# Kernel optimization log

Measured on AMD Instinct MI355X. Metric: run time of the kernel, lower is better.

Reference implementation:

```python
import jax, jax.numpy as jnp
import numpy as np

RCUT = 6.0      # cutoff radius
AXIS = 16       # axis_neuron
NORM = 64.0     # normalizer = avg_neighbors + 1 (precomputed stat)
EPS = 1e-15
NTYPES = 2


def _embed(h, W0, b0, W1, b1, W2, b2):
    # tiny per-type-pair embedding MLP: scalar sr -> C channels
    h = jnp.tanh(h @ W0 + b0)
    h = jnp.tanh(h @ W1 + b1)
    return jnp.tanh(h @ W2 + b2)


def _forward(coord_3N, box_33, srmean, srstd, xrsrstd, Gbias, Ebias,
             emb_W0, emb_b0, emb_W1, emb_b1, emb_W2, emb_b2,
             fit_W0, fit_b0, fit_W1, fit_b1, fit_W2, fit_b2, n1):
    N = coord_3N.shape[1]
    L = jnp.diagonal(box_33)  # orthorhombic box lengths (3,)
    # relative coords with minimum-image convention: x[d,i,j] = c[d,j] - c[d,i]
    x_3NM = coord_3N[:, None, :] - coord_3N[:, :, None]
    x_3NM = x_3NM - L[:, None, None] * jnp.round(x_3NM / L[:, None, None])
    eye = jnp.eye(N, dtype=bool)
    r_NM = jnp.sqrt(jnp.where(eye, 1.0, (x_3NM ** 2).sum(0)))  # diag masked for safe grad
    # smooth switching / r  (DeepPot-SE style sr)
    u = r_NM / RCUT
    sw = jnp.where((r_NM < RCUT) & (~eye), ((-6.0 * u + 15.0) * u - 10.0) * u ** 3 + 1.0, 0.0)
    sr_NM = sw / r_NM
    rsr_NM = sr_NM / r_NM
    idx = (0, n1, N)  # contiguous type boundaries (atoms sorted by type)
    rows_sr, rows_rsr, rows_emb = [], [], []
    for i in range(NTYPES):
        sr_i = sr_NM[idx[i]:idx[i + 1]]
        rows_sr.append(sr_i / srstd[i])
        rows_rsr.append(rsr_NM[idx[i]:idx[i + 1]] / xrsrstd[i])
        srn_i = (sr_i - srmean[i]) / srstd[i]
        blocks = []
        for j in range(NTYPES):
            p = NTYPES * i + j  # type-pair index
            blocks.append(_embed(srn_i[:, idx[j]:idx[j + 1], None],
                                 emb_W0[p], emb_b0[p], emb_W1[p], emb_b1[p], emb_W2[p], emb_b2[p]))
        rows_emb.append(jnp.concatenate(blocks, axis=1))
    srbias_NM = jnp.concatenate(rows_sr, axis=0)
    R_3NM = (jnp.concatenate(rows_rsr, axis=0)[None] + EPS) * x_3NM  # e3norm = 1
    embed_NMC = jnp.concatenate(rows_emb, axis=0)
    # weighted reductions over neighbor axis M (einsum avoids the 3*N*M*C temp)
    Ginv_NC = jnp.einsum('nm,nmc->nc', srbias_NM, embed_NMC) / NORM
    Geqv_3NC = jnp.einsum('dnm,nmc->dnc', R_3NM, embed_NMC) / NORM
    G_4NC = jnp.concatenate([(Ginv_NC + Gbias)[None], Geqv_3NC], axis=0)
    # equivariant outer-product descriptor: Feat[n,a,c] = sum_k G[k,n,c]*G[k,n,a]
    Feat_NX = jnp.einsum('knc,kna->nac', G_4NC, G_4NC[:, :, :AXIS]).reshape(N, -1)
    energy = jnp.zeros((), dtype=Feat_NX.dtype)
    for i in range(NTYPES):
        h = Feat_NX[idx[i]:idx[i + 1]]
        h = jnp.tanh(h @ fit_W0[i] + fit_b0[i])
        h = jnp.tanh(h @ fit_W1[i] + fit_b1[i])
        h = h @ fit_W2[i] + fit_b2[i]
        energy = energy + (h + Ebias[i]).sum()
    return energy


def setup_inputs() -> dict:
    key = jax.random.key(0)
    ks = jax.random.split(key, 20)
    N, N1, BOXL = 1024, 512, 20.0
    W = (16, 32, 64)
    X, F = AXIS * W[-1], 128

    def wt(k, shape, fan_in):
        return jax.random.normal(k, shape, jnp.float32) / np.float32(np.sqrt(fan_in))

    return {
        'coord_3N': jax.random.uniform(ks[0], (3, N), jnp.float32) * BOXL,
        'box_33': BOXL * jnp.eye(3, dtype=jnp.float32),
        'srmean': 0.1 * jax.random.uniform(ks[1], (NTYPES,), jnp.float32),
        'srstd': 0.5 + jax.random.uniform(ks[2], (NTYPES,), jnp.float32),
        'xrsrstd': 0.5 + jax.random.uniform(ks[3], (NTYPES,), jnp.float32),
        'Gbias': 0.1 * jax.random.normal(ks[4], (W[2],), jnp.float32),
        'Ebias': jax.random.normal(ks[5], (NTYPES,), jnp.float32),
        'emb_W0': wt(ks[6], (4, 1, W[0]), 1),
        'emb_b0': 0.1 * jax.random.normal(ks[7], (4, W[0]), jnp.float32),
        'emb_W1': wt(ks[8], (4, W[0], W[1]), W[0]),
        'emb_b1': 0.1 * jax.random.normal(ks[9], (4, W[1]), jnp.float32),
        'emb_W2': wt(ks[10], (4, W[1], W[2]), W[1]),
        'emb_b2': 0.1 * jax.random.normal(ks[11], (4, W[2]), jnp.float32),
        'fit_W0': wt(ks[12], (NTYPES, X, F), X),
        'fit_b0': 0.1 * jax.random.normal(ks[13], (NTYPES, F), jnp.float32),
        'fit_W1': wt(ks[14], (NTYPES, F, F), F),
        'fit_b1': 0.1 * jax.random.normal(ks[15], (NTYPES, F), jnp.float32),
        'fit_W2': wt(ks[16], (NTYPES, F, 1), F),
        'fit_b2': 0.1 * jax.random.normal(ks[17], (NTYPES, 1), jnp.float32),
        'n1': N1,
    }


def reference(coord_3N, box_33, srmean, srstd, xrsrstd, Gbias, Ebias,
              emb_W0, emb_b0, emb_W1, emb_b1, emb_W2, emb_b2,
              fit_W0, fit_b0, fit_W1, fit_b1, fit_W2, fit_b2, n1):
    return _forward(coord_3N, box_33, srmean, srstd, xrsrstd, Gbias, Ebias,
                    emb_W0, emb_b0, emb_W1, emb_b1, emb_W2, emb_b2,
                    fit_W0, fit_b0, fit_W1, fit_b1, fit_W2, fit_b2, n1)
```

## Files before the change

kernel.cpp:

```cpp
#include <hip/hip_runtime.h>

#define RCUT 6.0f

typedef _Float16 h2v __attribute__((ext_vector_type(2)));
typedef _Float16 h8  __attribute__((ext_vector_type(8)));
typedef float    f4  __attribute__((ext_vector_type(4)));

__device__ __forceinline__ float fast_tanh(float x) {
    float e = __expf(2.0f * x);
    return 1.0f - 2.0f * __builtin_amdgcn_rcpf(e + 1.0f);
}

__device__ __forceinline__ h2v pkh(float a, float b) {
#if __has_builtin(__builtin_amdgcn_cvt_pkrtz)
    union { __fp16 __attribute__((ext_vector_type(2))) r; h2v h; } u;
    u.r = __builtin_amdgcn_cvt_pkrtz(a, b);
    return u.h;
#else
    h2v r; r.x = (_Float16)a; r.y = (_Float16)b; return r;
#endif
}

__global__ __launch_bounds__(256, 2) void k_embed(
    const float* __restrict__ coord, const float* __restrict__ box,
    const float* __restrict__ srmean, const float* __restrict__ srstd,
    const float* __restrict__ xrsrstd, const float* __restrict__ Gbias,
    const float* __restrict__ eW0, const float* __restrict__ eb0,
    const float* __restrict__ eW1, const float* __restrict__ eb1,
    const float* __restrict__ eW2, const float* __restrict__ eb2,
    const int* __restrict__ n1p,
    const float* __restrict__ fW0, const float* __restrict__ fW1,
    h2v* __restrict__ feat, _Float16* __restrict__ W0ht,
    _Float16* __restrict__ W1ht, unsigned int* __restrict__ counter, int N)
{
    const int nb  = blockIdx.x;
    const int tid = threadIdx.x;
    const int NB  = N >> 1;

    __shared__ float s_w0[2][16], s_b0[2][16];
    __shared__ __align__(16) _Float16 s_srn[1024];
    __shared__ __align__(16) _Float16 s_cf[4][1024];
    __shared__ __align__(16) _Float16 s_h1[128][32];
    __shared__ __align__(16) _Float16 s_ef[4][4][64][8];
    __shared__ unsigned short s_nbr[1024];
    __shared__ float s_g4[2][256];
    __shared__ __align__(16) _Float16 w1t[2][32][24];
    __shared__ __align__(16) _Float16 w2t[2][64][40];
    __shared__ int s_wA[4], s_wB[4];

    if (nb >= NB) {
        const int b = nb - NB;
        if (b == 0 && tid == 0) *counter = 0u;
        float (*s_t)[33] = reinterpret_cast<float(*)[33]>(&s_ef[0][0][0][0]);
        if (b < 256) {
            int type = b >> 7, tb = b & 127;
            int ki = tb >> 2, ci = tb & 3;
            const float* src = fW0 + (size_t)type * 131072;
            int c = tid & 31, r0 = (tid >> 5) * 4;
            #pragma unroll
            for (int q = 0; q < 4; q++)
                s_t[r0 + q][c] = src[(size_t)(ki * 32 + r0 + q) * 128 + ci * 32 + c];
            __syncthreads();
            _Float16* dst = W0ht + (size_t)type * 131072;
            int kk = tid & 31, c0 = (tid >> 5) * 4;
            #pragma unroll
            for (int q = 0; q < 4; q++)
                dst[(size_t)(ci * 32 + c0 + q) * 1024 + ki * 32 + kk] = (_Float16)s_t[kk][c0 + q];
        } else {
            int b2v = b - 256, type = b2v >> 4, tb = b2v & 15;
            int ki = tb >> 2, ci = tb & 3;
            const float* src = fW1 + (size_t)type * 16384;
            int c = tid & 31, r0 = (tid >> 5) * 4;
            #pragma unroll
            for (int q = 0; q < 4; q++)
                s_t[r0 + q][c] = src[(size_t)(ki * 32 + r0 + q) * 128 + ci * 32 + c];
            __syncthreads();
            _Float16* dst = W1ht + (size_t)type * 16384;
            int kk = tid & 31, c0 = (tid >> 5) * 4;
            #pragma unroll
            for (int q = 0; q < 4; q++)
                dst[(size_t)(ci * 32 + c0 + q) * 128 + ki * 32 + kk] = (_Float16)s_t[kk][c0 + q];
        }
        return;
    }

    const int nA = 2 * nb, nBt = 2 * nb + 1;
    const int n1 = *n1p;
    const int ti = (nA >= n1) ? 1 : 0;
    const int wid = tid >> 6, lane = tid & 63;
    const int l15 = lane & 15, lk = lane >> 4;

    for (int t = tid; t < 32; t += 256) { int j = t >> 4, f = t & 15;
        s_w0[j][f] = eW0[(2 * ti + j) * 16 + f];
        s_b0[j][f] = eb0[(2 * ti + j) * 16 + f]; }
    for (int idx = tid; idx < 1024; idx += 256) {
        int j = idx >> 9, r = idx & 511, f = r >> 5, g = r & 31;
        w1t[j][g][f] = (_Float16)eW1[(2 * ti + j) * 512 + f * 32 + g];
    }
    for (int idx = tid; idx < 4096; idx += 256) {
        int j = idx >> 11, r = idx & 2047, g = r >> 6, c = r & 63;
        w2t[j][c][g] = (_Float16)eW2[(2 * ti + j) * 2048 + g * 64 + c];
    }
    float b1r[2][2], b2r[2][4];
    #pragma unroll
    for (int j = 0; j < 2; j++) {
        #pragma unroll
        for (int q = 0; q < 2; q++) b1r[j][q] = eb1[(2 * ti + j) * 32 + 16 * q + l15];
        #pragma unroll
        for (int q = 0; q < 4; q++) b2r[j][q] = eb2[(2 * ti + j) * 64 + 16 * q + l15];
    }

    const float Lx = box[0], Ly = box[4], Lz = box[8];
    const float iLx = 1.0f / Lx, iLy = 1.0f / Ly, iLz = 1.0f / Lz;
    const float xA = coord[nA], yA = coord[N + nA], zA = coord[2 * N + nA];
    const float xB = coord[nBt], yB = coord[N + nBt], zB = coord[2 * N + nBt];
    const float srm  = srmean[ti];
    const float isrs = 1.0f / srstd[ti];
    const float ixrs = 1.0f / xrsrstd[ti];

    unsigned long long balA[4], balB[4];
    {
        int wA = 0, wB = 0;
        const int mystart = wid * 256;
        #pragma unroll
        for (int r = 0; r < 4; r++) {
            int m = mystart + r * 64 + lane;
            float x = coord[m], y = coord[N + m], z = coord[2 * N + m];
            float ax = x - xA; ax -= Lx * rintf(ax * iLx);
            float ay = y - yA; ay -= Ly * rintf(ay * iLy);
            float az = z - zA; az -= Lz * rintf(az * iLz);
            float ra = ax * ax + ay * ay + az * az;
            float bx = x - xB; bx -= Lx * rintf(bx * iLx);
            float by = y - yB; by -= Ly * rintf(by * iLy);
            float bz = z - zB; bz -= Lz * rintf(bz * iLz);
            float rb = bx * bx + by * by + bz * bz;
            bool pA = (ra < RCUT * RCUT) && (m != nA);
            bool pB = (rb < RCUT * RCUT) && (m != nBt);
            balA[r] = __ballot(pA);
            balB[r] = __ballot(pB);
            wA += (int)__popcll(balA[r]);
            wB += (int)__popcll(balB[r]);
        }
        if (lane == 0) { s_wA[wid] = wA; s_wB[wid] = wB; }
    }
    __syncthreads();
    int cntA = s_wA[0] + s_wA[1] + s_wA[2] + s_wA[3];
    int cntB = s_wB[0] + s_wB[1] + s_wB[2] + s_wB[3];
    int cnt  = cntA + cntB;
    if (cnt > 1024) cnt = 1024;
    if (cntA > 1024) cntA = 1024;
    {
        int baseA = 0, baseB = cntA;
        for (int w = 0; w < wid; w++) { baseA += s_wA[w]; baseB += s_wB[w]; }
        const unsigned long long lt = (1ull << lane) - 1ull;
        const int mystart = wid * 256;
        #pragma unroll
        for (int r = 0; r < 4; r++) {
            int m = mystart + r * 64 + lane;
            float x = coord[m], y = coord[N + m], z = coord[2 * N + m];
            #pragma unroll
            for (int cc = 0; cc < 2; cc++) {
                unsigned long long bal = cc ? balB[r] : balA[r];
                int base = cc ? baseB : baseA;
                if ((bal >> lane) & 1ull) {
                    int pos = base + (int)__popcll(bal & lt);
                    if (pos < 1024) {
                        float dx = x - (cc ? xB : xA); dx -= Lx * rintf(dx * iLx);
                        float dy = y - (cc ? yB : yA); dy -= Ly * rintf(dy * iLy);
                        float dz = z - (cc ? zB : zA); dz -= Lz * rintf(dz * iLz);
                        float r2 = dx * dx + dy * dy + dz * dz;
                        float rr = sqrtf(r2);
                        float rinv = __builtin_amdgcn_rcpf(rr);
                        float u  = rr * (1.0f / RCUT);
                        float u3 = u * u * u;
                        float sw_ = ((-6.0f * u + 15.0f) * u - 10.0f) * u3 + 1.0f;
                        float sr  = sw_ * rinv;
                        float crs = sr * rinv * ixrs + 1e-15f;
                        s_srn[pos]   = (_Float16)((sr - srm) * isrs);
                        s_cf[0][pos] = (_Float16)(sr * isrs);
                        s_cf[1][pos] = (_Float16)(crs * dx);
                        s_cf[2][pos] = (_Float16)(crs * dy);
                        s_cf[3][pos] = (_Float16)(crs * dz);
                        s_nbr[pos]   = (unsigned short)m;
                    }
                }
                if (cc) baseB += (int)__popcll(bal);
                else    baseA += (int)__popcll(bal);
            }
        }
    }
    __syncthreads();
    const int ntiles = (cnt + 127) >> 7;
    for (int i = cnt + tid; i < ntiles * 128; i += 256) {
        s_srn[i] = (_Float16)0.0f; s_nbr[i] = 0;
        s_cf[0][i] = (_Float16)0.0f; s_cf[1][i] = (_Float16)0.0f;
        s_cf[2][i] = (_Float16)0.0f; s_cf[3][i] = (_Float16)0.0f;
    }
    __syncthreads();

    f4 gacc = {0.0f, 0.0f, 0.0f, 0.0f};
    const f4 zf4 = {0.0f, 0.0f, 0.0f, 0.0f};

    for (int t = 0; t < ntiles; t++) {
        const int t128 = t << 7;
        __syncthreads();

        #pragma unroll
        for (int mt2 = 0; mt2 < 2; mt2++) {
            const int mt = 2 * wid + mt2;
            const int row = 16 * mt + l15;
            const int rp = t128 + row;
            float srn = (float)s_srn[rp];
            int jr = (s_nbr[rp] >= n1) ? 1 : 0;
            h8 a = {};
            if (lk < 2) {
                const float* wp = &s_w0[jr][8 * lk];
                const float* bp = &s_b0[jr][8 * lk];
                #pragma unroll
                for (int q = 0; q < 8; q++)
                    a[q] = (_Float16)fast_tanh(fmaf(srn, wp[q], bp[q]));
            }
            #pragma unroll
            for (int nt1 = 0; nt1 < 2; nt1++) {
                const int c = 16 * nt1 + l15;
                h8 b0f = {}, b1f = {};
                if (lk < 2) {
                    b0f = *(const h8*)&w1t[0][c][8 * lk];
                    b1f = *(const h8*)&w1t[1][c][8 * lk];
                }
                f4 d0 = __builtin_amdgcn_mfma_f32_16x16x32_f16(a, b0f, zf4, 0, 0, 0);
                f4 d1 = __builtin_amdgcn_mfma_f32_16x16x32_f16(a, b1f, zf4, 0, 0, 0);
                #pragma unroll
                for (int r = 0; r < 4; r++) {
                    int gp = 16 * mt + 4 * lk + r;
                    bool is0 = (s_nbr[t128 + gp] < n1);
                    float hv = fast_tanh((is0 ? d0[r] : d1[r]) + (is0 ? b1r[0][nt1] : b1r[1][nt1]));
                    int e = 16 * nt1 + l15;
                    s_h1[gp][(((e >> 3) ^ ((gp >> 1) & 3)) << 3) + (e & 7)] = (_Float16)hv;
                }
            }
        }
        asm volatile("" ::: "memory");
        #pragma unroll
        for (int mt2 = 0; mt2 < 2; mt2++) {
            const int mt = 2 * wid + mt2;
            const int row = 16 * mt + l15;
            h8 a2 = *(const h8*)&s_h1[row][((lk ^ ((row >> 1) & 3)) << 3)];
            #pragma unroll
            for (int nt = 0; nt < 4; nt++) {
                const int c = 16 * nt + l15;
                h8 w20 = *(const h8*)&w2t[0][c][8 * lk];
                h8 w21 = *(const h8*)&w2t[1][c][8 * lk];
                f4 e0 = __builtin_amdgcn_mfma_f32_16x16x32_f16(a2, w20, zf4, 0, 0, 0);
                f4 e1 = __builtin_amdgcn_mfma_f32_16x16x32_f16(a2, w21, zf4, 0, 0, 0);
                #pragma unroll
                for (int r = 0; r < 4; r++) {
                    int gp = 16 * mt + 4 * lk + r;
                    bool is0 = (s_nbr[t128 + gp] < n1);
                    float ev = fast_tanh((is0 ? e0[r] : e1[r]) + (is0 ? b2r[0][nt] : b2r[1][nt]));
                    s_ef[nt][gp >> 5][l15 + 16 * ((gp & 31) >> 3)][gp & 7] = (_Float16)ev;
                }
            }
        }
        __syncthreads();

        #pragma unroll
        for (int ks = 0; ks < 4; ks++) {
            const int s = t128 + 32 * ks;
            h8 ac = {};
            if (l15 < 8) {
                const bool rowA = l15 < 4;
                const int  cr   = rowA ? l15 : (l15 - 4);
                const bool allA = (s + 31) < cntA;
                const bool allB = s >= cntA;
                if ((allA && rowA) || (allB && !rowA)) {
                    ac = *(const h8*)&s_cf[cr][s + 8 * lk];
                } else if (!allA && !allB) {
                    #pragma unroll
                    for (int r = 0; r < 8; r++) {
                        int p = s + 8 * lk + r;
                        bool isA = p < cntA;
                        if (isA == rowA) ac[r] = s_cf[cr][p];
                    }
                }
            }
            h8 eb = *(const h8*)&s_ef[wid][ks][lane][0];
            gacc = __builtin_amdgcn_mfma_f32_16x16x32_f16(ac, eb, gacc, 0, 0, 0);
        }
    }

    if (lk < 2) {
        float* sg = &s_g4[lk][0];
        #pragma unroll
        for (int r = 0; r < 4; r++) {
            float gv = gacc[r] * (1.0f / 64.0f);
            if (r == 0) gv += Gbias[16 * wid + l15];
            sg[r * 64 + 16 * wid + l15] = gv;
        }
    }
    __syncthreads();
    #pragma unroll
    for (int at = 0; at < 2; at++) {
        const float* sg = &s_g4[at][0];
        h2v* outp = feat + (size_t)(2 * nb + at) * 512;
        #pragma unroll
        for (int q = 0; q < 2; q++) {
            int o2 = tid + 256 * q;
            int a = o2 >> 5, c = (2 * o2) & 63;
            float ga0 = sg[a],       ga1 = sg[64 + a];
            float ga2 = sg[128 + a], ga3 = sg[192 + a];
            float s0 = ga0 * sg[c];
            s0 = fmaf(ga1, sg[64 + c],  s0);
            s0 = fmaf(ga2, sg[128 + c], s0);
            s0 = fmaf(ga3, sg[192 + c], s0);
            float s1 = ga0 * sg[c + 1];
            s1 = fmaf(ga1, sg[64 + c + 1],  s1);
            s1 = fmaf(ga2, sg[128 + c + 1], s1);
            s1 = fmaf(ga3, sg[192 + c + 1], s1);
            outp[o2] = pkh(s0, s1);
        }
    }
}

__global__ __launch_bounds__(512) void k_fit(
    const _Float16* __restrict__ featf, const _Float16* __restrict__ W0ht,
    const _Float16* __restrict__ W1ht,
    const float* __restrict__ b0, const float* __restrict__ b1,
    const float* __restrict__ W2, const float* __restrict__ b2,
    const float* __restrict__ Ebias, const int* __restrict__ n1p,
    unsigned int* __restrict__ counter, float* __restrict__ slots,
    float* __restrict__ out)
{
    __shared__ float s_red[4][2][16][64];
    __shared__ __align__(16) _Float16 s_hd[16][128];
    __shared__ float s_sum[16][32];

    const int tid = threadIdx.x;
    const int lane = tid & 63, w = tid >> 6;
    const int kq = w >> 1, ch = w & 1;
    const int l15 = lane & 15, lk = lane >> 4;
    const int n0 = blockIdx.x * 16;
    const int ia = (n0 >= *n1p) ? 1 : 0;
    const f4 zf4 = {0.0f, 0.0f, 0.0f, 0.0f};

    const _Float16* Ap = featf + (size_t)(n0 + l15) * 1024 + kq * 256;
    const _Float16* B0 = W0ht + (size_t)ia * 131072 + kq * 256;
    f4 acc[4] = {zf4, zf4, zf4, zf4};
    #pragma unroll
    for (int ks = 0; ks < 8; ks++) {
        h8 a = *(const h8*)(Ap + ks * 32 + 8 * lk);
        #pragma unroll
        for (int nt = 0; nt < 4; nt++) {
            const int c = ch * 64 + nt * 16 + l15;
            h8 b = *(const h8*)(B0 + (size_t)c * 1024 + ks * 32 + 8 * lk);
            acc[nt] = __builtin_amdgcn_mfma_f32_16x16x32_f16(a, b, acc[nt], 0, 0, 0);
        }
    }
    #pragma unroll
    for (int nt = 0; nt < 4; nt++)
        #pragma unroll
        for (int r = 0; r < 4; r++)
            s_red[kq][ch][4 * lk + r][nt * 16 + l15] = acc[nt][r];
    __syncthreads();

    {
        const int row = tid >> 5, c0 = (tid & 31) * 4;
        const int chh = c0 >> 6, cl = c0 & 63;
        f4 v = *(const f4*)&s_red[0][chh][row][cl];
        v += *(const f4*)&s_red[1][chh][row][cl];
        v += *(const f4*)&s_red[2][chh][row][cl];
        v += *(const f4*)&s_red[3][chh][row][cl];
        #pragma unroll
        for (int q = 0; q < 4; q++) {
            int c = c0 + q;
            float h = fast_tanh(v[q] + b0[ia * 128 + c]);
            s_hd[row][(((c >> 3) ^ row) << 3) + (c & 7)] = (_Float16)h;
        }
    }
    __syncthreads();

    f4 acc1[4] = {zf4, zf4, zf4, zf4};
    {
        h8 a = *(const h8*)&s_hd[l15][(((4 * kq + lk) ^ l15) & 15) << 3];
        const _Float16* B1 = W1ht + (size_t)ia * 16384 + kq * 32;
        #pragma unroll
        for (int nt = 0; nt < 4; nt++) {
            const int c = ch * 64 + nt * 16 + l15;
            h8 b = *(const h8*)(B1 + (size_t)c * 128 + 8 * lk);
            acc1[nt] = __builtin_amdgcn_mfma_f32_16x16x32_f16(a, b, zf4, 0, 0, 0);
        }
    }
    #pragma unroll
    for (int nt = 0; nt < 4; nt++)
        #pragma unroll
        for (int r = 0; r < 4; r++)
            s_red[kq][ch][4 * lk + r][nt * 16 + l15] = acc1[nt][r];
    __syncthreads();

    {
        const int row = tid >> 5, c0 = (tid & 31) * 4;
        const int chh = c0 >> 6, cl = c0 & 63;
        f4 v = *(const f4*)&s_red[0][chh][row][cl];
        v += *(const f4*)&s_red[1][chh][row][cl];
        v += *(const f4*)&s_red[2][chh][row][cl];
        v += *(const f4*)&s_red[3][chh][row][cl];
        float pv = 0.0f;
        #pragma unroll
        for (int q = 0; q < 4; q++) {
            int c = c0 + q;
            pv += fast_tanh(v[q] + b1[ia * 128 + c]) * W2[ia * 128 + c];
        }
        s_sum[row][tid & 31] = pv;
    }
    __syncthreads();
    if (w == 0) {
        const int row = lane >> 2, g = lane & 3;
        float s = 0.0f;
        #pragma unroll
        for (int i = 0; i < 8; i++) s += s_sum[row][8 * g + i];
        s += __shfl_xor(s, 1);  s += __shfl_xor(s, 2);
        s += __shfl_xor(s, 4);  s += __shfl_xor(s, 8);
        s += __shfl_xor(s, 16); s += __shfl_xor(s, 32);
        if (lane == 0) {
            float e = s + 16.0f * (b2[ia] + Ebias[ia]);
            slots[blockIdx.x] = e;
            __threadfence();
            unsigned int old = atomicAdd(counter, 1u);
            if (old == 63u) {
                __threadfence();
                float tot = 0.0f;
                for (int i = 0; i < 64; i++)
                    tot += __hip_atomic_load(&slots[i], __ATOMIC_RELAXED, __HIP_MEMORY_SCOPE_AGENT);
                out[0] = tot;
            }
        }
    }
}

extern "C" void kernel_launch(void* const* d_in, const int* in_sizes, int n_in,
                              void* d_out, int out_size, void* d_ws, size_t ws_size,
                              hipStream_t stream) {
    const float* coord   = (const float*)d_in[0];
    const float* box     = (const float*)d_in[1];
    const float* srmean  = (const float*)d_in[2];
    const float* srstd   = (const float*)d_in[3];
    const float* xrsrstd = (const float*)d_in[4];
    const float* Gbias   = (const float*)d_in[5];
    const float* Ebias   = (const float*)d_in[6];
    const float* eW0     = (const float*)d_in[7];
    const float* eb0     = (const float*)d_in[8];
    const float* eW1     = (const float*)d_in[9];
    const float* eb1     = (const float*)d_in[10];
    const float* eW2     = (const float*)d_in[11];
    const float* eb2     = (const float*)d_in[12];
    const float* fW0     = (const float*)d_in[13];
    const float* fb0     = (const float*)d_in[14];
    const float* fW1     = (const float*)d_in[15];
    const float* fb1     = (const float*)d_in[16];
    const float* fW2     = (const float*)d_in[17];
    const float* fb2     = (const float*)d_in[18];
    const int*   n1p     = (const int*)d_in[19];

    const int N = in_sizes[0] / 3;
    h2v*      featbuf = (h2v*)d_ws;
    _Float16* W0ht = (_Float16*)((char*)d_ws + (size_t)2 * 1024 * 1024);
    _Float16* W1ht = W0ht + 2 * 131072;
    char* tail = (char*)d_ws + (size_t)(2 * 1024 + 512 + 64) * 1024;
    unsigned int* counter = (unsigned int*)tail;
    float*        slots   = (float*)(tail + 64);

    k_embed<<<N / 2 + 288, 256, 0, stream>>>(coord, box, srmean, srstd, xrsrstd,
                                             Gbias, eW0, eb0, eW1, eb1, eW2, eb2,
                                             n1p, fW0, fW1, featbuf, W0ht, W1ht,
                                             counter, N);
    k_fit<<<N / 16, 512, 0, stream>>>((const _Float16*)featbuf, W0ht, W1ht,
                                      fb0, fb1, fW2, fb2, Ebias, n1p,
                                      counter, slots, (float*)d_out);
}
```

Before: 39.37 us.

## Process one atom per block and accumulate G in registers instead of MFMA

```diff
diff --git a/kernel.cpp b/kernel.cpp
--- a/kernel.cpp
+++ b/kernel.cpp
@@ -21,7 +21,7 @@
 #endif
 }
 
-__global__ __launch_bounds__(256, 2) void k_embed(
+__global__ __launch_bounds__(256, 4) void k_embed(
     const float* __restrict__ coord, const float* __restrict__ box,
     const float* __restrict__ srmean, const float* __restrict__ srstd,
     const float* __restrict__ xrsrstd, const float* __restrict__ Gbias,
@@ -33,25 +33,23 @@
     h2v* __restrict__ feat, _Float16* __restrict__ W0ht,
     _Float16* __restrict__ W1ht, unsigned int* __restrict__ counter, int N)
 {
-    const int nb  = blockIdx.x;
     const int tid = threadIdx.x;
-    const int NB  = N >> 1;
 
     __shared__ float s_w0[2][16], s_b0[2][16];
-    __shared__ __align__(16) _Float16 s_srn[1024];
-    __shared__ __align__(16) _Float16 s_cf[4][1024];
+    __shared__ __align__(16) _Float16 s_srn[512];
+    __shared__ __align__(16) _Float16 s_cf[4][512];
     __shared__ __align__(16) _Float16 s_h1[128][32];
-    __shared__ __align__(16) _Float16 s_ef[4][4][64][8];
-    __shared__ unsigned short s_nbr[1024];
-    __shared__ float s_g4[2][256];
+    __shared__ unsigned short s_nbr[512];
+    __shared__ float s_g[4][4][64];
+    __shared__ float s_g4[256];
     __shared__ __align__(16) _Float16 w1t[2][32][24];
     __shared__ __align__(16) _Float16 w2t[2][64][40];
-    __shared__ int s_wA[4], s_wB[4];
-
-    if (nb >= NB) {
-        const int b = nb - NB;
+    __shared__ int s_wcnt[4];
+
+    if (blockIdx.x >= (unsigned)N) {
+        const int b = blockIdx.x - N;
         if (b == 0 && tid == 0) *counter = 0u;
-        float (*s_t)[33] = reinterpret_cast<float(*)[33]>(&s_ef[0][0][0][0]);
+        float (*s_t)[33] = reinterpret_cast<float(*)[33]>(&s_h1[0][0]);
         if (b < 256) {
             int type = b >> 7, tb = b & 127;
             int ki = tb >> 2, ci = tb & 3;
@@ -84,9 +82,9 @@
         return;
     }
 
-    const int nA = 2 * nb, nBt = 2 * nb + 1;
+    const int n  = blockIdx.x;
     const int n1 = *n1p;
-    const int ti = (nA >= n1) ? 1 : 0;
+    const int ti = (n >= n1) ? 1 : 0;
     const int wid = tid >> 6, lane = tid & 63;
     const int l15 = lane & 15, lk = lane >> 4;
 
@@ -112,81 +110,62 @@
 
     const float Lx = box[0], Ly = box[4], Lz = box[8];
     const float iLx = 1.0f / Lx, iLy = 1.0f / Ly, iLz = 1.0f / Lz;
-    const float xA = coord[nA], yA = coord[N + nA], zA = coord[2 * N + nA];
-    const float xB = coord[nBt], yB = coord[N + nBt], zB = coord[2 * N + nBt];
+    const float xn = coord[n], yn = coord[N + n], zn = coord[2 * N + n];
     const float srm  = srmean[ti];
     const float isrs = 1.0f / srstd[ti];
     const float ixrs = 1.0f / xrsrstd[ti];
 
-    unsigned long long balA[4], balB[4];
-    {
-        int wA = 0, wB = 0;
+    unsigned long long bal[4];
+    {
+        int wc = 0;
         const int mystart = wid * 256;
         #pragma unroll
         for (int r = 0; r < 4; r++) {
             int m = mystart + r * 64 + lane;
-            float x = coord[m], y = coord[N + m], z = coord[2 * N + m];
-            float ax = x - xA; ax -= Lx * rintf(ax * iLx);
-            float ay = y - yA; ay -= Ly * rintf(ay * iLy);
-            float az = z - zA; az -= Lz * rintf(az * iLz);
-            float ra = ax * ax + ay * ay + az * az;
-            float bx = x - xB; bx -= Lx * rintf(bx * iLx);
-            float by = y - yB; by -= Ly * rintf(by * iLy);
-            float bz = z - zB; bz -= Lz * rintf(bz * iLz);
-            float rb = bx * bx + by * by + bz * bz;
-            bool pA = (ra < RCUT * RCUT) && (m != nA);
-            bool pB = (rb < RCUT * RCUT) && (m != nBt);
-            balA[r] = __ballot(pA);
-            balB[r] = __ballot(pB);
-            wA += (int)__popcll(balA[r]);
-            wB += (int)__popcll(balB[r]);
-        }
-        if (lane == 0) { s_wA[wid] = wA; s_wB[wid] = wB; }
-    }
-    __syncthreads();
-    int cntA = s_wA[0] + s_wA[1] + s_wA[2] + s_wA[3];
-    int cntB = s_wB[0] + s_wB[1] + s_wB[2] + s_wB[3];
-    int cnt  = cntA + cntB;
-    if (cnt > 1024) cnt = 1024;
-    if (cntA > 1024) cntA = 1024;
-    {
-        int baseA = 0, baseB = cntA;
-        for (int w = 0; w < wid; w++) { baseA += s_wA[w]; baseB += s_wB[w]; }
+            float dx = coord[m] - xn;         dx -= Lx * rintf(dx * iLx);
+            float dy = coord[N + m] - yn;     dy -= Ly * rintf(dy * iLy);
+            float dz = coord[2 * N + m] - zn; dz -= Lz * rintf(dz * iLz);
+            float r2 = dx * dx + dy * dy + dz * dz;
+            bool pred = (r2 < RCUT * RCUT) && (m != n);
+            bal[r] = __ballot(pred);
+            wc += (int)__popcll(bal[r]);
+        }
+        if (lane == 0) s_wcnt[wid] = wc;
+    }
+    __syncthreads();
+    int cnt = s_wcnt[0] + s_wcnt[1] + s_wcnt[2] + s_wcnt[3];
+    if (cnt > 512) cnt = 512;
+    {
+        int base = 0;
+        for (int w = 0; w < wid; w++) base += s_wcnt[w];
         const unsigned long long lt = (1ull << lane) - 1ull;
         const int mystart = wid * 256;
         #pragma unroll
         for (int r = 0; r < 4; r++) {
             int m = mystart + r * 64 + lane;
-            float x = coord[m], y = coord[N + m], z = coord[2 * N + m];
-            #pragma unroll
-            for (int cc = 0; cc < 2; cc++) {
-                unsigned long long bal = cc ? balB[r] : balA[r];
-                int base = cc ? baseB : baseA;
-                if ((bal >> lane) & 1ull) {
-                    int pos = base + (int)__popcll(bal & lt);
-                    if (pos < 1024) {
-                        float dx = x - (cc ? xB : xA); dx -= Lx * rintf(dx * iLx);
-                        float dy = y - (cc ? yB : yA); dy -= Ly * rintf(dy * iLy);
-                        float dz = z - (cc ? zB : zA); dz -= Lz * rintf(dz * iLz);
-                        float r2 = dx * dx + dy * dy + dz * dz;
-                        float rr = sqrtf(r2);
-                        float rinv = __builtin_amdgcn_rcpf(rr);
-                        float u  = rr * (1.0f / RCUT);
-                        float u3 = u * u * u;
-                        float sw_ = ((-6.0f * u + 15.0f) * u - 10.0f) * u3 + 1.0f;
-                        float sr  = sw_ * rinv;
-                        float crs = sr * rinv * ixrs + 1e-15f;
-                        s_srn[pos]   = (_Float16)((sr - srm) * isrs);
-                        s_cf[0][pos] = (_Float16)(sr * isrs);
-                        s_cf[1][pos] = (_Float16)(crs * dx);
-                        s_cf[2][pos] = (_Float16)(crs * dy);
-                        s_cf[3][pos] = (_Float16)(crs * dz);
-                        s_nbr[pos]   = (unsigned short)m;
-                    }
+            if ((bal[r] >> lane) & 1ull) {
+                int pos = base + (int)__popcll(bal[r] & lt);
+                if (pos < 512) {
+                    float dx = coord[m] - xn;         dx -= Lx * rintf(dx * iLx);
+                    float dy = coord[N + m] - yn;     dy -= Ly * rintf(dy * iLy);
+                    float dz = coord[2 * N + m] - zn; dz -= Lz * rintf(dz * iLz);
+                    float r2 = dx * dx + dy * dy + dz * dz;
+                    float rr = sqrtf(r2);
+                    float rinv = __builtin_amdgcn_rcpf(rr);
+                    float u  = rr * (1.0f / RCUT);
+                    float u3 = u * u * u;
+                    float sw_ = ((-6.0f * u + 15.0f) * u - 10.0f) * u3 + 1.0f;
+                    float sr  = sw_ * rinv;
+                    float crs = sr * rinv * ixrs + 1e-15f;
+                    s_srn[pos]   = (_Float16)((sr - srm) * isrs);
+                    s_cf[0][pos] = (_Float16)(sr * isrs);
+                    s_cf[1][pos] = (_Float16)(crs * dx);
+                    s_cf[2][pos] = (_Float16)(crs * dy);
+                    s_cf[3][pos] = (_Float16)(crs * dz);
+                    s_nbr[pos]   = (unsigned short)m;
                 }
-                if (cc) baseB += (int)__popcll(bal);
-                else    baseA += (int)__popcll(bal);
-            }
+            }
+            base += (int)__popcll(bal[r]);
         }
     }
     __syncthreads();
@@ -198,13 +177,11 @@
     }
     __syncthreads();
 
-    f4 gacc = {0.0f, 0.0f, 0.0f, 0.0f};
     const f4 zf4 = {0.0f, 0.0f, 0.0f, 0.0f};
+    float gk[4][4] = {};
 
     for (int t = 0; t < ntiles; t++) {
         const int t128 = t << 7;
-        __syncthreads();
-
         #pragma unroll
         for (int mt2 = 0; mt2 < 2; mt2++) {
             const int mt = 2 * wid + mt2;
@@ -220,6 +197,11 @@
                 for (int q = 0; q < 8; q++)
                     a[q] = (_Float16)fast_tanh(fmaf(srn, wp[q], bp[q]));
             }
+            int j_r[4];
+            #pragma unroll
+            for (int r = 0; r < 4; r++)
+                j_r[r] = (s_nbr[t128 + 16 * mt + 4 * lk + r] >= n1) ? 1 : 0;
+
             #pragma unroll
             for (int nt1 = 0; nt1 < 2; nt1++) {
                 const int c = 16 * nt1 + l15;
@@ -233,90 +215,74 @@
                 #pragma unroll
                 for (int r = 0; r < 4; r++) {
                     int gp = 16 * mt + 4 * lk + r;
-                    bool is0 = (s_nbr[t128 + gp] < n1);
-                    float hv = fast_tanh((is0 ? d0[r] : d1[r]) + (is0 ? b1r[0][nt1] : b1r[1][nt1]));
+                    float hv = fast_tanh((j_r[r] ? d1[r] : d0[r]) + (j_r[r] ? b1r[1][nt1] : b1r[0][nt1]));
                     int e = 16 * nt1 + l15;
                     s_h1[gp][(((e >> 3) ^ ((gp >> 1) & 3)) << 3) + (e & 7)] = (_Float16)hv;
                 }
             }
-        }
-        asm volatile("" ::: "memory");
-        #pragma unroll
-        for (int mt2 = 0; mt2 < 2; mt2++) {
-            const int mt = 2 * wid + mt2;
-            const int row = 16 * mt + l15;
+            asm volatile("" ::: "memory");
+
             h8 a2 = *(const h8*)&s_h1[row][((lk ^ ((row >> 1) & 3)) << 3)];
+            float cfv[4][4];
+            #pragma unroll
+            for (int k = 0; k < 4; k++) {
+                #pragma unroll
+                for (int r = 0; r < 4; r++)
+                    cfv[k][r] = (float)s_cf[k][t128 + 16 * mt + 4 * lk + r];
+            }
             #pragma unroll
             for (int nt = 0; nt < 4; nt++) {
-                const int c = 16 * nt + l15;
-                h8 w20 = *(const h8*)&w2t[0][c][8 * lk];
-                h8 w21 = *(const h8*)&w2t[1][c][8 * lk];
+                h8 w20 = *(const h8*)&w2t[0][16 * nt + l15][8 * lk];
+                h8 w21 = *(const h8*)&w2t[1][16 * nt + l15][8 * lk];
                 f4 e0 = __builtin_amdgcn_mfma_f32_16x16x32_f16(a2, w20, zf4, 0, 0, 0);
                 f4 e1 = __builtin_amdgcn_mfma_f32_16x16x32_f16(a2, w21, zf4, 0, 0, 0);
                 #pragma unroll
                 for (int r = 0; r < 4; r++) {
-                    int gp = 16 * mt + 4 * lk + r;
-                    bool is0 = (s_nbr[t128 + gp] < n1);
-                    float ev = fast_tanh((is0 ? e0[r] : e1[r]) + (is0 ? b2r[0][nt] : b2r[1][nt]));
-                    s_ef[nt][gp >> 5][l15 + 16 * ((gp & 31) >> 3)][gp & 7] = (_Float16)ev;
+                    float ev = fast_tanh((j_r[r] ? e1[r] : e0[r]) + (j_r[r] ? b2r[1][nt] : b2r[0][nt]));
+                    #pragma unroll
+                    for (int k = 0; k < 4; k++)
+                        gk[k][nt] = fmaf(cfv[k][r], ev, gk[k][nt]);
                 }
             }
         }
-        __syncthreads();
-
-        #pragma unroll
-        for (int ks = 0; ks < 4; ks++) {
-            const int s = t128 + 32 * ks;
-            h8 ac = {};
-            if (l15 < 8) {
-                const bool rowA = l15 < 4;
-                const int  cr   = rowA ? l15 : (l15 - 4);
-                const bool allA = (s + 31) < cntA;
-                const bool allB = s >= cntA;
-                if ((allA && rowA) || (allB && !rowA)) {
-                    ac = *(const h8*)&s_cf[cr][s + 8 * lk];
-                } else if (!allA && !allB) {
-                    #pragma unroll
-                    for (int r = 0; r < 8; r++) {
-                        int p = s + 8 * lk + r;
-                        bool isA = p < cntA;
-                        if (isA == rowA) ac[r] = s_cf[cr][p];
-                    }
-                }
-            }
-            h8 eb = *(const h8*)&s_ef[wid][ks][lane][0];
-            gacc = __builtin_amdgcn_mfma_f32_16x16x32_f16(ac, eb, gacc, 0, 0, 0);
-        }
-    }
-
-    if (lk < 2) {
-        float* sg = &s_g4[lk][0];
-        #pragma unroll
-        for (int r = 0; r < 4; r++) {
-            float gv = gacc[r] * (1.0f / 64.0f);
-            if (r == 0) gv += Gbias[16 * wid + l15];
-            sg[r * 64 + 16 * wid + l15] = gv;
-        }
-    }
-    __syncthreads();
+    }
+
     #pragma unroll
-    for (int at = 0; at < 2; at++) {
-        const float* sg = &s_g4[at][0];
-        h2v* outp = feat + (size_t)(2 * nb + at) * 512;
+    for (int k = 0; k < 4; k++) {
+        #pragma unroll
+        for (int nt = 0; nt < 4; nt++) {
+            float v = gk[k][nt];
+            v += __shfl_xor(v, 16);
+            v += __shfl_xor(v, 32);
+            if (lane < 16) s_g[wid][k][nt * 16 + lane] = v;
+        }
+    }
+    __syncthreads();
+    {
+        int k = tid >> 6, c = tid & 63;
+        float g = (s_g[0][k][c] + s_g[1][k][c]) + (s_g[2][k][c] + s_g[3][k][c]);
+        g *= (1.0f / 64.0f);
+        if (k == 0) g += Gbias[c];
+        s_g4[k * 64 + c] = g;
+    }
+    __syncthreads();
+
+    {
+        h2v* outp = feat + (size_t)n * 512;
         #pragma unroll
         for (int q = 0; q < 2; q++) {
             int o2 = tid + 256 * q;
             int a = o2 >> 5, c = (2 * o2) & 63;
-            float ga0 = sg[a],       ga1 = sg[64 + a];
-            float ga2 = sg[128 + a], ga3 = sg[192 + a];
-            float s0 = ga0 * sg[c];
-            s0 = fmaf(ga1, sg[64 + c],  s0);
-            s0 = fmaf(ga2, sg[128 + c], s0);
-            s0 = fmaf(ga3, sg[192 + c], s0);
-            float s1 = ga0 * sg[c + 1];
-            s1 = fmaf(ga1, sg[64 + c + 1],  s1);
-            s1 = fmaf(ga2, sg[128 + c + 1], s1);
-            s1 = fmaf(ga3, sg[192 + c + 1], s1);
+            float ga0 = s_g4[a],       ga1 = s_g4[64 + a];
+            float ga2 = s_g4[128 + a], ga3 = s_g4[192 + a];
+            float s0 = ga0 * s_g4[c];
+            s0 = fmaf(ga1, s_g4[64 + c],  s0);
+            s0 = fmaf(ga2, s_g4[128 + c], s0);
+            s0 = fmaf(ga3, s_g4[192 + c], s0);
+            float s1 = ga0 * s_g4[c + 1];
+            s1 = fmaf(ga1, s_g4[64 + c + 1],  s1);
+            s1 = fmaf(ga2, s_g4[128 + c + 1], s1);
+            s1 = fmaf(ga3, s_g4[192 + c + 1], s1);
             outp[o2] = pkh(s0, s1);
         }
     }
@@ -469,10 +435,10 @@
     unsigned int* counter = (unsigned int*)tail;
     float*        slots   = (float*)(tail + 64);
 
-    k_embed<<<N / 2 + 288, 256, 0, stream>>>(coord, box, srmean, srstd, xrsrstd,
-                                             Gbias, eW0, eb0, eW1, eb1, eW2, eb2,
-                                             n1p, fW0, fW1, featbuf, W0ht, W1ht,
-                                             counter, N);
+    k_embed<<<N + 288, 256, 0, stream>>>(coord, box, srmean, srstd, xrsrstd,
+                                         Gbias, eW0, eb0, eW1, eb1, eW2, eb2,
+                                         n1p, fW0, fW1, featbuf, W0ht, W1ht,
+                                         counter, N);
     k_fit<<<N / 16, 512, 0, stream>>>((const _Float16*)featbuf, W0ht, W1ht,
                                       fb0, fb1, fW2, fb2, Ebias, n1p,
                                       counter, slots, (float*)d_out);
```

Result: no change. 39.59 us (+0.6%).
